# Kernel tuning notes

Hardware: AMD Instinct MI355X
Metric: run time of the kernel (lower is better)

The kernel has to match this reference:

```python
import jax, jax.numpy as jnp
import numpy as np

EPS = 1e-6

def _ln(x, g, b):
    mu = jnp.mean(x, axis=-1, keepdims=True)
    var = jnp.mean(jnp.square(x - mu), axis=-1, keepdims=True)
    return (x - mu) * jax.lax.rsqrt(var + EPS) * g + b

def setup_inputs() -> dict:
    key = jax.random.key(0)
    ks = jax.random.split(key, 8)
    B, S, D, H, HD, F = 4, 1024, 1024, 16, 64, 4096
    s = 0.02
    return {
        "hidden_state": jax.random.normal(ks[0], (B, S, D), jnp.float32),
        "mask": jnp.ones((B, S), jnp.int32),
        "Wq": jax.random.normal(ks[1], (H, D, HD), jnp.float32) * s,
        "bq": jnp.zeros((H, HD), jnp.float32),
        "Wk": jax.random.normal(ks[2], (H, D, HD), jnp.float32) * s,
        "bk": jnp.zeros((H, HD), jnp.float32),
        "Wv": jax.random.normal(ks[3], (H, D, HD), jnp.float32) * s,
        "bv": jnp.zeros((H, HD), jnp.float32),
        "Wo": jax.random.normal(ks[4], (D, D), jnp.float32) * s,
        "bo": jnp.zeros((D,), jnp.float32),
        "ln1_g": jnp.ones((D,), jnp.float32),
        "ln1_b": jnp.zeros((D,), jnp.float32),
        "ln2_g": jnp.ones((D,), jnp.float32),
        "ln2_b": jnp.zeros((D,), jnp.float32),
        "W1": jax.random.normal(ks[5], (D, F), jnp.float32) * s,
        "b1": jnp.zeros((F,), jnp.float32),
        "W2": jax.random.normal(ks[6], (F, D), jnp.float32) * s,
        "b2": jnp.zeros((D,), jnp.float32),
    }

def reference(hidden_state, mask, Wq, bq, Wk, bk, Wv, bv, Wo, bo,
              ln1_g, ln1_b, ln2_g, ln2_b, W1, b1, W2, b2):
    # Pre-norm
    x1 = _ln(hidden_state, ln1_g, ln1_b)  # [B,S,D]
    # Per-head projections stacked over head axis h
    q = jnp.einsum('bsd,hdk->bhsk', x1, Wq) + bq[:, None, :]
    k = jnp.einsum('bsd,hdk->bhsk', x1, Wk) + bk[:, None, :]
    v = jnp.einsum('bsd,hdk->bhsk', x1, Wv) + bv[:, None, :]
    head_dim = q.shape[-1]
    scores = jnp.einsum('bhqk,bhsk->bhqs', q, k) / jnp.sqrt(jnp.float32(head_dim))
    scores = jnp.where(mask[:, None, None, :] == 0, jnp.float32(-1e9), scores)
    w = jax.nn.softmax(scores, axis=-1)
    attn = jnp.einsum('bhqs,bhsk->bhqk', w, v)  # [B,H,S,HD]
    B, H, S, HD = attn.shape
    attn = attn.transpose(0, 2, 1, 3).reshape(B, S, H * HD)  # concat heads
    attn = attn @ Wo + bo
    h = attn + hidden_state
    x2 = _ln(h, ln2_g, ln2_b)
    ff = jax.nn.gelu(x2 @ W1 + b1, approximate=False) @ W2 + b2
    return ff + h
```

## Files before the change

### kernel.cpp

```cpp
#include <hip/hip_runtime.h>

typedef __bf16 bf16;
typedef __bf16 bf16x4 __attribute__((ext_vector_type(4)));
typedef __bf16 bf16x8 __attribute__((ext_vector_type(8)));
typedef float  f32x4  __attribute__((ext_vector_type(4)));

#define F32X4_ZERO ((f32x4){0.f, 0.f, 0.f, 0.f})

__device__ __forceinline__ f32x4 mfma16(bf16x8 a, bf16x8 b, f32x4 c) {
  return __builtin_amdgcn_mfma_f32_16x16x32_bf16(a, b, c, 0, 0, 0);
}

__device__ __forceinline__ void gld16(const void* g, void* l) {
  __builtin_amdgcn_global_load_lds((const __attribute__((address_space(1))) void*)g,
                                   (__attribute__((address_space(3))) void*)l, 16, 0, 0);
}

__device__ __forceinline__ float gelu_f(float u) {
  return 0.5f * u * (1.0f + erff(u * 0.70710678118654752f));
}

__device__ __forceinline__ bf16x8 frag_ld(const bf16* base, int row, int c16) {
  return *(const bf16x8*)((const char*)base + row * 128 + (((c16) ^ (row & 7)) << 4));
}

__device__ __forceinline__ bf16x8 frag_ld32(const bf16* base, int row, int c16) {
  return *(const bf16x8*)((const char*)base + row * 64 + ((c16 ^ ((row >> 1) & 3)) << 4));
}
#define WAITB(N) asm volatile("s_waitcnt vmcnt(" #N ")\ns_barrier" ::: "memory")

__global__ void transpose2(const float* __restrict__ src, size_t sBatch, int sStride,
                           bf16* __restrict__ dst, size_t dBatch, int dStride) {
  __shared__ bf16 t[32][33];
  src += (size_t)blockIdx.z * sBatch;
  dst += (size_t)blockIdx.z * dBatch;
  int c0 = blockIdx.x * 32, r0 = blockIdx.y * 32;
#pragma unroll
  for (int i = 0; i < 4; i++) {
    int r = threadIdx.y + i * 8;
    t[r][threadIdx.x] = (bf16)src[(size_t)(r0 + r) * sStride + c0 + threadIdx.x];
  }
  __syncthreads();
#pragma unroll
  for (int i = 0; i < 4; i++) {
    int c = threadIdx.y + i * 8;
    dst[(size_t)(c0 + c) * dStride + r0 + threadIdx.x] = t[threadIdx.x][c];
  }
}

__global__ __launch_bounds__(256) void ln_rows(const float* __restrict__ in,
                                               const float* __restrict__ gam,
                                               const float* __restrict__ bet,
                                               bf16* __restrict__ out) {
  int row = blockIdx.x, tid = threadIdx.x;
  f32x4 x = *(const f32x4*)(in + (size_t)row * 1024 + tid * 4);
  float s = 0.f, q = 0.f;
#pragma unroll
  for (int j = 0; j < 4; j++) { s += x[j]; q += x[j] * x[j]; }
#pragma unroll
  for (int o = 1; o < 64; o <<= 1) {
    s += __shfl_xor(s, o, 64);
    q += __shfl_xor(q, o, 64);
  }
  __shared__ float red[8];
  if ((tid & 63) == 0) { red[(tid >> 6) * 2] = s; red[(tid >> 6) * 2 + 1] = q; }
  __syncthreads();
  s = red[0] + red[2] + red[4] + red[6];
  q = red[1] + red[3] + red[5] + red[7];
  float mean = s * (1.f / 1024.f);
  float var  = q * (1.f / 1024.f) - mean * mean;
  float inv  = rsqrtf(var + 1e-6f);
  bf16x4 o;
#pragma unroll
  for (int j = 0; j < 4; j++) {
    int c = tid * 4 + j;
    o[j] = (bf16)((x[j] - mean) * inv * gam[c] + bet[c]);
  }
  *(bf16x4*)(out + (size_t)row * 1024 + tid * 4) = o;
}

enum { EPI_WO = 0, EPI_GELU = 1, EPI_ACC0 = 2, EPI_ACC = 3, EPI_FINAL = 4 };

__global__ __launch_bounds__(512) void pipe256x128_gelu(
    const bf16* __restrict__ A, const bf16* __restrict__ BT, const float* __restrict__ bias,
    int N, bf16* __restrict__ outb) {
  int tid = threadIdx.x, lane = tid & 63, wv = tid >> 6;
  int bid = blockIdx.x;
  int xcd = bid & 7, idx = bid >> 3;
  int mg = xcd >> 1, ng = xcd & 1;
  int m0 = (mg * 4 + (idx >> 4)) * 256;
  int n0 = (ng * 16 + (idx & 15)) * 128;
  int wrow = (wv >> 1) * 64, wcol = (wv & 1) * 64;
  __shared__ __align__(16) bf16 lds[3][12288];
  f32x4 acc[4][4];
#pragma unroll
  for (int a = 0; a < 4; a++)
#pragma unroll
    for (int n = 0; n < 4; n++) acc[a][n] = F32X4_ZERO;

  constexpr int K = 1024, nk = K / 32;
  int rin = lane >> 2;
  int sbc = ((lane & 3) ^ ((lane >> 3) & 3)) * 16;
  auto stage = [&](int slot, int k0) {
#pragma unroll
    for (int j = 0; j < 3; j++) {
      int c = wv * 3 + j;
      if (c < 16)
        gld16((const char*)A + ((size_t)(m0 + c * 16 + rin) * K + k0) * 2 + sbc,
              (char*)lds[slot] + c * 1024);
      else
        gld16((const char*)BT + ((size_t)(n0 + (c - 16) * 16 + rin) * K + k0) * 2 + sbc,
              (char*)lds[slot] + c * 1024);
    }
  };

  stage(0, 0); stage(1, 32);
#pragma unroll 1
  for (int t = 0; t < nk; t++) {
    if (t < nk - 1) WAITB(3);
    else            WAITB(0);
    if (t + 2 < nk) stage((t + 2) % 3, (t + 2) * 32);
    const bf16* As = lds[t % 3];
    const bf16* Bs = lds[t % 3] + 8192;
    int c16 = lane >> 4;
    bf16x8 af[4], bfr[4];
#pragma unroll
    for (int mf = 0; mf < 4; mf++)
      af[mf] = frag_ld32(As, wrow + mf * 16 + (lane & 15), c16);
#pragma unroll
    for (int nf = 0; nf < 4; nf++)
      bfr[nf] = frag_ld32(Bs, wcol + nf * 16 + (lane & 15), c16);
#pragma unroll
    for (int mf = 0; mf < 4; mf++)
#pragma unroll
      for (int nf = 0; nf < 4; nf++)
        acc[mf][nf] = mfma16(af[mf], bfr[nf], acc[mf][nf]);
  }
#pragma unroll
  for (int mf = 0; mf < 4; mf++)
#pragma unroll
    for (int nf = 0; nf < 4; nf++)
#pragma unroll
      for (int i = 0; i < 4; i++) {
        int row = m0 + wrow + mf * 16 + ((lane >> 4) << 2) + i;
        int col = n0 + wcol + nf * 16 + (lane & 15);
        outb[(size_t)row * N + col] = (bf16)gelu_f(acc[mf][nf][i] + bias[col]);
      }
}

template <int EPI, int K, int NTL>
__global__ __launch_bounds__(256) void pipe128(
    const bf16* __restrict__ A, const bf16* __restrict__ BT, const float* __restrict__ bias,
    int N,
    const float* __restrict__ resid, float* __restrict__ facc,
    bf16* __restrict__ outb, float* __restrict__ outf) {
  int tid = threadIdx.x, lane = tid & 63, wv = tid >> 6;
  int bid = blockIdx.x + (blockIdx.y << 3);
  int xcd = bid & 7, idx = bid >> 3;
  int m0 = (xcd * 4 + (idx >> NTL)) * 128;
  int n0 = (idx & ((1 << NTL) - 1)) * 128;
  int wrow = (wv >> 1) * 64, wcol = (wv & 1) * 64;
  __shared__ __align__(16) bf16 lds[3][8192];
  f32x4 acc[4][4];
#pragma unroll
  for (int a = 0; a < 4; a++)
#pragma unroll
    for (int n = 0; n < 4; n++) acc[a][n] = F32X4_ZERO;

  constexpr int nk = K / 32;
  int rin = lane >> 2;
  int sbc = ((lane & 3) ^ ((lane >> 3) & 3)) * 16;
  auto stage = [&](int slot, int k0) {
#pragma unroll
    for (int j = 0; j < 4; j++) {
      int c = wv * 4 + j;
      if (c < 8)
        gld16((const char*)A + ((size_t)(m0 + c * 16 + rin) * K + k0) * 2 + sbc,
              (char*)lds[slot] + c * 1024);
      else
        gld16((const char*)BT + ((size_t)(n0 + (c - 8) * 16 + rin) * K + k0) * 2 + sbc,
              (char*)lds[slot] + c * 1024);
    }
  };

  stage(0, 0); stage(1, 32);
#pragma unroll 1
  for (int t = 0; t < nk; t++) {
    if (t < nk - 1) WAITB(4);
    else            WAITB(0);
    if (t + 2 < nk) stage((t + 2) % 3, (t + 2) * 32);
    const bf16* As = lds[t % 3];
    const bf16* Bs = lds[t % 3] + 4096;
    int c16 = lane >> 4;
    bf16x8 af[4], bfr[4];
#pragma unroll
    for (int mf = 0; mf < 4; mf++)
      af[mf] = frag_ld32(As, wrow + mf * 16 + (lane & 15), c16);
#pragma unroll
    for (int nf = 0; nf < 4; nf++)
      bfr[nf] = frag_ld32(Bs, wcol + nf * 16 + (lane & 15), c16);
#pragma unroll
    for (int mf = 0; mf < 4; mf++)
#pragma unroll
      for (int nf = 0; nf < 4; nf++)
        acc[mf][nf] = mfma16(af[mf], bfr[nf], acc[mf][nf]);
  }
#pragma unroll
  for (int mf = 0; mf < 4; mf++)
#pragma unroll
    for (int nf = 0; nf < 4; nf++)
#pragma unroll
      for (int i = 0; i < 4; i++) {
        int row = m0 + wrow + mf * 16 + ((lane >> 4) << 2) + i;
        int col = n0 + wcol + nf * 16 + (lane & 15);
        size_t idx2 = (size_t)row * N + col;
        float v = acc[mf][nf][i];
        if constexpr (EPI == EPI_WO) {
          outf[idx2] = v + bias[col] + resid[idx2];
        } else if constexpr (EPI == EPI_GELU) {
          outb[idx2] = (bf16)gelu_f(v + bias[col]);
        } else if constexpr (EPI == EPI_ACC0) {
          facc[idx2] = v;
        } else if constexpr (EPI == EPI_ACC) {
          facc[idx2] += v;
        } else {
          outf[idx2] = facc[idx2] + v + bias[col] + resid[idx2];
        }
      }
}

__global__ __launch_bounds__(256) void qkv_pipe(
    const bf16* __restrict__ x1,
    const bf16* __restrict__ WqT, const bf16* __restrict__ WkT, const bf16* __restrict__ WvT,
    const float* __restrict__ bq, const float* __restrict__ bk, const float* __restrict__ bv,
    bf16* __restrict__ qo, bf16* __restrict__ ko, bf16* __restrict__ vto) {
  int tid = threadIdx.x, lane = tid & 63, wv = tid >> 6;
  int z = blockIdx.z;
  const bf16* BT; const float* bias;
  if (z == 0)      { BT = WqT; bias = bq; }
  else if (z == 1) { BT = WkT; bias = bk; }
  else             { BT = WvT; bias = bv; }
  int bid = blockIdx.x + (blockIdx.y << 3);
  int xcd = bid & 7, idx = bid >> 3;
  int m0 = (xcd * 4 + (idx >> 3)) * 128, n0 = (idx & 7) * 128;
  int wrow = (wv >> 1) * 64, wcol = (wv & 1) * 64;
  __shared__ __align__(16) bf16 lds[3][8192];
  f32x4 acc[4][4];
#pragma unroll
  for (int a = 0; a < 4; a++)
#pragma unroll
    for (int n = 0; n < 4; n++) acc[a][n] = F32X4_ZERO;

  constexpr int K = 1024, nk = K / 32;
  int rin = lane >> 2;
  int sbc = ((lane & 3) ^ ((lane >> 3) & 3)) * 16;
  auto stage = [&](int slot, int k0) {
#pragma unroll
    for (int j = 0; j < 4; j++) {
      int c = wv * 4 + j;
      if (c < 8)
        gld16((const char*)x1 + ((size_t)(m0 + c * 16 + rin) * K + k0) * 2 + sbc,
              (char*)lds[slot] + c * 1024);
      else
        gld16((const char*)BT + ((size_t)(n0 + (c - 8) * 16 + rin) * K + k0) * 2 + sbc,
              (char*)lds[slot] + c * 1024);
    }
  };

  stage(0, 0); stage(1, 32);
#pragma unroll 1
  for (int t = 0; t < nk; t++) {
    if (t < nk - 1) WAITB(4);
    else            WAITB(0);
    if (t + 2 < nk) stage((t + 2) % 3, (t + 2) * 32);
    const bf16* As = lds[t % 3];
    const bf16* Bs = lds[t % 3] + 4096;
    int c16 = lane >> 4;
    bf16x8 af[4], bfr[4];
#pragma unroll
    for (int mf = 0; mf < 4; mf++)
      af[mf] = frag_ld32(As, wrow + mf * 16 + (lane & 15), c16);
#pragma unroll
    for (int nf = 0; nf < 4; nf++)
      bfr[nf] = frag_ld32(Bs, wcol + nf * 16 + (lane & 15), c16);
#pragma unroll
    for (int mf = 0; mf < 4; mf++)
#pragma unroll
      for (int nf = 0; nf < 4; nf++)
        acc[mf][nf] = mfma16(af[mf], bfr[nf], acc[mf][nf]);
  }
#pragma unroll
  for (int mf = 0; mf < 4; mf++)
#pragma unroll
    for (int nf = 0; nf < 4; nf++)
#pragma unroll
      for (int i = 0; i < 4; i++) {
        int row  = m0 + wrow + mf * 16 + ((lane >> 4) << 2) + i;
        int ncol = n0 + wcol + nf * 16 + (lane & 15);
        int bb = row >> 10, s = row & 1023, head = ncol >> 6, d = ncol & 63;
        size_t bh = (size_t)bb * 16 + head;
        float v = acc[mf][nf][i] + bias[ncol];
        if (z == 0)      qo[(bh * 1024 + s) * 64 + d] = (bf16)(v * 0.125f);
        else if (z == 1) ko[(bh * 1024 + s) * 64 + d] = (bf16)v;
        else             vto[(bh * 64 + d) * 1024 + s] = (bf16)v;
      }
}

__global__ __launch_bounds__(512) void attn_flash(
    const bf16* __restrict__ qb, const bf16* __restrict__ kb, const bf16* __restrict__ vtb,
    const int* __restrict__ mask, bf16* __restrict__ attnC) {
  int tid = threadIdx.x, lane = tid & 63, wv = tid >> 6;
  int wgid = blockIdx.x;
  int nid  = (wgid & 7) * 64 + (wgid >> 3);
  int qblk = nid & 7, h = (nid >> 3) & 15, b = nid >> 7;
  int qrow0 = qblk * 128 + wv * 16;

  __shared__ float smask[1024];
  __shared__ __align__(16) bf16 kt[2][64 * 64];
  __shared__ __align__(16) bf16 vt[2][64 * 64];
  __shared__ __align__(16) bf16 pb[8][16][72];
  for (int i = tid; i < 1024; i += 512) smask[i] = mask[b * 1024 + i] ? 0.f : -1e9f;

  size_t bh = (size_t)b * 16 + h;
  const bf16* qp = qb + (bh * 1024 + qrow0) * 64;
  bf16x8 qa[2];
#pragma unroll
  for (int kc = 0; kc < 2; kc++)
    qa[kc] = *(const bf16x8*)(qp + (lane & 15) * 64 + kc * 32 + (lane >> 4) * 8);

  const bf16* kp = kb + bh * 1024 * 64;
  const bf16* vp = vtb + bh * 64 * 1024;
  bf16* myp = &pb[wv][0][0];

  bf16x8 vone;
#pragma unroll
  for (int j = 0; j < 8; j++) vone[j] = (bf16)1.0f;

  f32x4 ssum = F32X4_ZERO;
  f32x4 oacc[4];
#pragma unroll
  for (int i = 0; i < 4; i++) oacc[i] = F32X4_ZERO;

  int srl = lane >> 3;
  int sbc = ((lane & 7) ^ srl) * 16;
  auto stage = [&](int buf, int t2) {
    int key0n = t2 * 64;
#pragma unroll
    for (int j = 0; j < 2; j++) {
      int c = wv * 2 + j;
      if (c < 8) {
        int row = c * 8 + srl;
        gld16((const char*)kp + ((size_t)(key0n + row) * 64) * 2 + sbc,
              (char*)kt[buf] + c * 1024);
      } else {
        int row = (c - 8) * 8 + srl;
        gld16((const char*)vp + ((size_t)row * 1024 + key0n) * 2 + sbc,
              (char*)vt[buf] + (c - 8) * 1024);
      }
    }
  };

  stage(0, 0);
  __syncthreads();

  for (int t = 0; t < 16; t++) {
    int cur = t & 1;
    if (t < 15) stage(cur ^ 1, t + 1);
    const bf16* kcur = kt[cur];
    const bf16* vcur = vt[cur];
    int key0 = t * 64;
    f32x4 st[4];
    __builtin_amdgcn_s_setprio(1);
#pragma unroll
    for (int nt = 0; nt < 4; nt++) {
      st[nt] = F32X4_ZERO;
#pragma unroll
      for (int kc = 0; kc < 2; kc++) {
        bf16x8 kf = frag_ld(kcur, nt * 16 + (lane & 15), kc * 4 + (lane >> 4));
        st[nt] = mfma16(qa[kc], kf, st[nt]);
      }
    }
    __builtin_amdgcn_s_setprio(0);
#pragma unroll
    for (int nt = 0; nt < 4; nt++) {
      float ms = smask[key0 + nt * 16 + (lane & 15)] - 8.0f;
#pragma unroll
      for (int i = 0; i < 4; i++) st[nt][i] = __expf(st[nt][i] + ms);
    }
#pragma unroll
    for (int nt = 0; nt < 4; nt++)
#pragma unroll
      for (int i = 0; i < 4; i++)
        myp[((lane >> 4) * 4 + i) * 72 + nt * 16 + (lane & 15)] = (bf16)st[nt][i];
    __builtin_amdgcn_s_setprio(1);
#pragma unroll
    for (int kc = 0; kc < 2; kc++) {
      bf16x8 pa = *(const bf16x8*)(myp + (lane & 15) * 72 + kc * 32 + (lane >> 4) * 8);
      ssum = mfma16(pa, vone, ssum);
#pragma unroll
      for (int dn = 0; dn < 4; dn++) {
        bf16x8 vf = frag_ld(vcur, dn * 16 + (lane & 15), kc * 4 + (lane >> 4));
        oacc[dn] = mfma16(pa, vf, oacc[dn]);
      }
    }
    __builtin_amdgcn_s_setprio(0);
    __syncthreads();
  }
#pragma unroll
  for (int i = 0; i < 4; i++) {
    float inv = 1.0f / ssum[i];
    int row = qrow0 + ((lane >> 4) << 2) + i;
#pragma unroll
    for (int dn = 0; dn < 4; dn++)
      attnC[(size_t)(b * 1024 + row) * 1024 + h * 64 + dn * 16 + (lane & 15)] =
          (bf16)(oacc[dn][i] * inv);
  }
}

template <int EPI, int K>
__global__ __launch_bounds__(256) void gemm_bt(
    const bf16* __restrict__ A, const bf16* __restrict__ BT, const float* __restrict__ bias,
    int N,
    const float* __restrict__ resid, float* __restrict__ facc,
    bf16* __restrict__ outb, float* __restrict__ outf) {
  int tid = threadIdx.x, lane = tid & 63, wv = tid >> 6;
  int m0 = blockIdx.y * 128, n0 = blockIdx.x * 128;
  int wrow = (wv >> 1) * 64, wcol = (wv & 1) * 64;
  __shared__ __align__(16) bf16 lA[2][128 * 64];
  __shared__ __align__(16) bf16 lB[2][128 * 64];
  f32x4 acc[4][4];
#pragma unroll
  for (int a = 0; a < 4; a++)
#pragma unroll
    for (int n = 0; n < 4; n++) acc[a][n] = F32X4_ZERO;

  int cbs = ((lane & 7) ^ (lane >> 3)) * 16;
  auto stage = [&](int buf, int k0) {
#pragma unroll
    for (int s = 0; s < 4; s++) {
      int c = s * 4 + wv;
      int row = c * 8 + (lane >> 3);
      gld16((const char*)A  + ((size_t)(m0 + row) * K + k0) * 2 + cbs,
            (char*)lA[buf] + c * 1024);
      gld16((const char*)BT + ((size_t)(n0 + row) * K + k0) * 2 + cbs,
            (char*)lB[buf] + c * 1024);
    }
  };

  constexpr int nk = K >> 6;
  stage(0, 0);
  __syncthreads();
#pragma unroll 1
  for (int t = 0; t < nk; t++) {
    int cur = t & 1;
    if (t + 1 < nk) stage(cur ^ 1, (t + 1) * 64);
#pragma unroll
    for (int kc = 0; kc < 2; kc++) {
      int c16 = kc * 4 + (lane >> 4);
      bf16x8 af[4], bfr[4];
#pragma unroll
      for (int mf = 0; mf < 4; mf++)
        af[mf] = frag_ld(lA[cur], wrow + mf * 16 + (lane & 15), c16);
#pragma unroll
      for (int nf = 0; nf < 4; nf++)
        bfr[nf] = frag_ld(lB[cur], wcol + nf * 16 + (lane & 15), c16);
#pragma unroll
      for (int mf = 0; mf < 4; mf++)
#pragma unroll
        for (int nf = 0; nf < 4; nf++)
          acc[mf][nf] = mfma16(af[mf], bfr[nf], acc[mf][nf]);
    }
    __syncthreads();
  }
#pragma unroll
  for (int mf = 0; mf < 4; mf++)
#pragma unroll
    for (int nf = 0; nf < 4; nf++)
#pragma unroll
      for (int i = 0; i < 4; i++) {
        int row = m0 + wrow + mf * 16 + ((lane >> 4) << 2) + i;
        int col = n0 + wcol + nf * 16 + (lane & 15);
        size_t idx2 = (size_t)row * N + col;
        float v = acc[mf][nf][i];
        if constexpr (EPI == EPI_WO) {
          outf[idx2] = v + bias[col] + resid[idx2];
        } else if constexpr (EPI == EPI_GELU) {
          outb[idx2] = (bf16)gelu_f(v + bias[col]);
        } else if constexpr (EPI == EPI_ACC0) {
          facc[idx2] = v;
        } else if constexpr (EPI == EPI_ACC) {
          facc[idx2] += v;
        } else {
          outf[idx2] = facc[idx2] + v + bias[col] + resid[idx2];
        }
      }
}

extern "C" void kernel_launch(void* const* d_in, const int* in_sizes, int n_in,
                              void* d_out, int out_size, void* d_ws, size_t ws_size,
                              hipStream_t stream) {
  const float* hidden = (const float*)d_in[0];
  const int*   mask   = (const int*)d_in[1];
  const float* Wq = (const float*)d_in[2];
  const float* bq = (const float*)d_in[3];
  const float* Wk = (const float*)d_in[4];
  const float* bk = (const float*)d_in[5];
  const float* Wv = (const float*)d_in[6];
  const float* bv = (const float*)d_in[7];
  const float* Wo = (const float*)d_in[8];
  const float* bo = (const float*)d_in[9];
  const float* ln1g = (const float*)d_in[10];
  const float* ln1b = (const float*)d_in[11];
  const float* ln2g = (const float*)d_in[12];
  const float* ln2b = (const float*)d_in[13];
  const float* W1 = (const float*)d_in[14];
  const float* b1 = (const float*)d_in[15];
  const float* W2 = (const float*)d_in[16];
  const float* b2 = (const float*)d_in[17];
  float* out = (float*)d_out;

  char* ws = (char*)d_ws;
  const size_t MB = 1ull << 20;
  dim3 tb(32, 8);
  const size_t HB = 64 * 1024;

  if (ws_size >= 96 * MB) {
    bf16* x1    = (bf16*)(ws + 0 * MB);
    bf16* attnC = x1;
    bf16* x2    = x1;
    bf16* qbuf  = (bf16*)(ws + 8 * MB);
    bf16* W1T   = qbuf;
    bf16* kbuf  = (bf16*)(ws + 16 * MB);
    bf16* W2T   = kbuf;
    bf16* vtbuf = (bf16*)(ws + 24 * MB);
    float* hbuf = (float*)(ws + 32 * MB);
    bf16* WqT   = (bf16*)(ws + 48 * MB);
    bf16* WkT   = (bf16*)(ws + 50 * MB);
    bf16* WvT   = (bf16*)(ws + 52 * MB);
    bf16* WoT   = (bf16*)(ws + 54 * MB);
    bf16* gbuf  = (bf16*)(ws + 56 * MB);

    transpose2<<<dim3(2, 32, 16), tb, 0, stream>>>(Wq, HB, 64, WqT, HB, 1024);
    transpose2<<<dim3(2, 32, 16), tb, 0, stream>>>(Wk, HB, 64, WkT, HB, 1024);
    transpose2<<<dim3(2, 32, 16), tb, 0, stream>>>(Wv, HB, 64, WvT, HB, 1024);
    transpose2<<<dim3(32, 32, 1), tb, 0, stream>>>(Wo, 0, 1024, WoT, 0, 1024);
    ln_rows<<<4096, 256, 0, stream>>>(hidden, ln1g, ln1b, x1);
    qkv_pipe<<<dim3(8, 32, 3), 256, 0, stream>>>(x1, WqT, WkT, WvT, bq, bk, bv,
                                                 qbuf, kbuf, vtbuf);
    attn_flash<<<512, 512, 0, stream>>>(qbuf, kbuf, vtbuf, mask, attnC);
    pipe128<EPI_WO, 1024, 3><<<dim3(8, 32), 256, 0, stream>>>(attnC, WoT, bo, 1024,
                                                              hidden, nullptr, nullptr, hbuf);
    ln_rows<<<4096, 256, 0, stream>>>(hbuf, ln2g, ln2b, x2);
    transpose2<<<dim3(128, 32, 1), tb, 0, stream>>>(W1, 0, 4096, W1T, 0, 1024);
    transpose2<<<dim3(32, 128, 1), tb, 0, stream>>>(W2, 0, 1024, W2T, 0, 4096);
    pipe256x128_gelu<<<512, 512, 0, stream>>>(x2, W1T, b1, 4096, gbuf);
    pipe128<EPI_WO, 4096, 3><<<dim3(8, 32), 256, 0, stream>>>(gbuf, W2T, b2, 1024,
                                                              hbuf, nullptr, nullptr, out);
  } else {
    bf16* x1     = (bf16*)(ws + 0 * MB);
    bf16* attnC  = x1;
    bf16* x2     = x1;
    bf16* qbuf   = (bf16*)(ws + 8 * MB);
    bf16* W1Tc   = (bf16*)(ws + 8 * MB);
    bf16* W2Tc   = (bf16*)(ws + 10 * MB);
    bf16* gchunk = (bf16*)(ws + 12 * MB);
    bf16* kbuf   = (bf16*)(ws + 16 * MB);
    bf16* vtbuf  = (bf16*)(ws + 24 * MB);
    float* hbuf  = (float*)(ws + 16 * MB);
    bf16* WqT    = (bf16*)(ws + 32 * MB);
    bf16* WkT    = (bf16*)(ws + 34 * MB);
    bf16* WvT    = (bf16*)(ws + 36 * MB);
    bf16* WoT    = (bf16*)(ws + 38 * MB);
    float* outacc = (float*)(ws + 40 * MB);

    transpose2<<<dim3(2, 32, 16), tb, 0, stream>>>(Wq, HB, 64, WqT, HB, 1024);
    transpose2<<<dim3(2, 32, 16), tb, 0, stream>>>(Wk, HB, 64, WkT, HB, 1024);
    transpose2<<<dim3(2, 32, 16), tb, 0, stream>>>(Wv, HB, 64, WvT, HB, 1024);
    transpose2<<<dim3(32, 32, 1), tb, 0, stream>>>(Wo, 0, 1024, WoT, 0, 1024);
    ln_rows<<<4096, 256, 0, stream>>>(hidden, ln1g, ln1b, x1);
    qkv_pipe<<<dim3(8, 32, 3), 256, 0, stream>>>(x1, WqT, WkT, WvT, bq, bk, bv,
                                                 qbuf, kbuf, vtbuf);
    attn_flash<<<512, 512, 0, stream>>>(qbuf, kbuf, vtbuf, mask, attnC);
    pipe128<EPI_WO, 1024, 3><<<dim3(8, 32), 256, 0, stream>>>(attnC, WoT, bo, 1024,
                                                              hidden, nullptr, nullptr, hbuf);
    ln_rows<<<4096, 256, 0, stream>>>(hbuf, ln2g, ln2b, x2);

    for (int c = 0; c < 8; c++) {
      transpose2<<<dim3(16, 32, 1), tb, 0, stream>>>(W1 + c * 512, 0, 4096,
                                                     W1Tc, 0, 1024);
      transpose2<<<dim3(32, 16, 1), tb, 0, stream>>>(W2 + (size_t)c * 512 * 1024, 0, 1024,
                                                     W2Tc, 0, 512);
      gemm_bt<EPI_GELU, 1024><<<dim3(4, 32), 256, 0, stream>>>(x2, W1Tc, b1 + c * 512, 512,
                                                               nullptr, nullptr, gchunk, nullptr);
      if (c == 0)
        gemm_bt<EPI_ACC0, 512><<<dim3(8, 32), 256, 0, stream>>>(gchunk, W2Tc, b2, 1024,
                                                                nullptr, outacc, nullptr, nullptr);
      else if (c < 7)
        gemm_bt<EPI_ACC, 512><<<dim3(8, 32), 256, 0, stream>>>(gchunk, W2Tc, b2, 1024,
                                                               nullptr, outacc, nullptr, nullptr);
      else
        gemm_bt<EPI_FINAL, 512><<<dim3(8, 32), 256, 0, stream>>>(gchunk, W2Tc, b2, 1024,
                                                                 hbuf, outacc, nullptr, out);
    }
  }

  (void)in_sizes; (void)n_in; (void)out_size;
}
```

Measured before the change: 223.0 us.

## Use 256x128 QKV GEMM tiles, deepen pipe128 prefetch, precompute load offsets

Replaces the 128x128 QKV projection kernel with a 512-thread 256x128 tile variant, mirroring the FFN1 kernel, to raise operand reuse per block. The pipe128 GEMMs used for Wo and W2 gain a DEPTH template parameter and now prefetch three stages ahead with four LDS slots to hide more global latency. All GEMM kernels precompute their global source pointers and swizzled LDS fragment offsets once, then advance pointers incrementally, which cuts per-iteration address arithmetic. The trade-off is more LDS per block and fewer QKV blocks, which may reduce occupancy.

```diff
diff --git a/kernel.cpp b/kernel.cpp
--- a/kernel.cpp
+++ b/kernel.cpp
@@ -24,8 +24,8 @@
   return *(const bf16x8*)((const char*)base + row * 128 + (((c16) ^ (row & 7)) << 4));
 }
 
-__device__ __forceinline__ bf16x8 frag_ld32(const bf16* base, int row, int c16) {
-  return *(const bf16x8*)((const char*)base + row * 64 + ((c16 ^ ((row >> 1) & 3)) << 4));
+__device__ __forceinline__ int fo32(int row, int c16) {
+  return row * 64 + ((c16 ^ ((row >> 1) & 3)) << 4);
 }
 #define WAITB(N) asm volatile("s_waitcnt vmcnt(" #N ")\ns_barrier" ::: "memory")
 
@@ -87,9 +87,8 @@
   int tid = threadIdx.x, lane = tid & 63, wv = tid >> 6;
   int bid = blockIdx.x;
   int xcd = bid & 7, idx = bid >> 3;
-  int mg = xcd >> 1, ng = xcd & 1;
-  int m0 = (mg * 4 + (idx >> 4)) * 256;
-  int n0 = (ng * 16 + (idx & 15)) * 128;
+  int m0 = ((xcd >> 1) * 4 + (idx >> 4)) * 256;
+  int n0 = ((xcd & 1) * 16 + (idx & 15)) * 128;
   int wrow = (wv >> 1) * 64, wcol = (wv & 1) * 64;
   __shared__ __align__(16) bf16 lds[3][12288];
   f32x4 acc[4][4];
@@ -101,35 +100,40 @@
   constexpr int K = 1024, nk = K / 32;
   int rin = lane >> 2;
   int sbc = ((lane & 3) ^ ((lane >> 3) & 3)) * 16;
-  auto stage = [&](int slot, int k0) {
+  const char* gsrc[3]; int ldof[3];
+#pragma unroll
+  for (int j = 0; j < 3; j++) {
+    int c = wv * 3 + j;
+    if (c < 16) gsrc[j] = (const char*)A  + ((size_t)(m0 + c * 16 + rin) * K) * 2 + sbc;
+    else        gsrc[j] = (const char*)BT + ((size_t)(n0 + (c - 16) * 16 + rin) * K) * 2 + sbc;
+    ldof[j] = c * 1024;
+  }
+  auto stage = [&](int slot) {
 #pragma unroll
     for (int j = 0; j < 3; j++) {
-      int c = wv * 3 + j;
-      if (c < 16)
-        gld16((const char*)A + ((size_t)(m0 + c * 16 + rin) * K + k0) * 2 + sbc,
-              (char*)lds[slot] + c * 1024);
-      else
-        gld16((const char*)BT + ((size_t)(n0 + (c - 16) * 16 + rin) * K + k0) * 2 + sbc,
-              (char*)lds[slot] + c * 1024);
+      gld16(gsrc[j], (char*)lds[slot] + ldof[j]);
+      gsrc[j] += 64;
     }
   };
-
-  stage(0, 0); stage(1, 32);
+  int c16 = lane >> 4;
+  int foA[4], foB[4];
+#pragma unroll
+  for (int mf = 0; mf < 4; mf++) foA[mf] = fo32(wrow + mf * 16 + (lane & 15), c16);
+#pragma unroll
+  for (int nf = 0; nf < 4; nf++) foB[nf] = 16384 + fo32(wcol + nf * 16 + (lane & 15), c16);
+
+  stage(0); stage(1);
 #pragma unroll 1
   for (int t = 0; t < nk; t++) {
     if (t < nk - 1) WAITB(3);
     else            WAITB(0);
-    if (t + 2 < nk) stage((t + 2) % 3, (t + 2) * 32);
-    const bf16* As = lds[t % 3];
-    const bf16* Bs = lds[t % 3] + 8192;
-    int c16 = lane >> 4;
+    if (t + 2 < nk) stage((t + 2) % 3);
+    const char* sb = (const char*)lds[t % 3];
     bf16x8 af[4], bfr[4];
 #pragma unroll
-    for (int mf = 0; mf < 4; mf++)
-      af[mf] = frag_ld32(As, wrow + mf * 16 + (lane & 15), c16);
-#pragma unroll
-    for (int nf = 0; nf < 4; nf++)
-      bfr[nf] = frag_ld32(Bs, wcol + nf * 16 + (lane & 15), c16);
+    for (int mf = 0; mf < 4; mf++) af[mf] = *(const bf16x8*)(sb + foA[mf]);
+#pragma unroll
+    for (int nf = 0; nf < 4; nf++) bfr[nf] = *(const bf16x8*)(sb + foB[nf]);
 #pragma unroll
     for (int mf = 0; mf < 4; mf++)
 #pragma unroll
@@ -148,7 +152,90 @@
       }
 }
 
-template <int EPI, int K, int NTL>
+__global__ __launch_bounds__(512) void qkv_pipe256(
+    const bf16* __restrict__ x1,
+    const bf16* __restrict__ WqT, const bf16* __restrict__ WkT, const bf16* __restrict__ WvT,
+    const float* __restrict__ bq, const float* __restrict__ bk, const float* __restrict__ bv,
+    bf16* __restrict__ qo, bf16* __restrict__ ko, bf16* __restrict__ vto) {
+  int tid = threadIdx.x, lane = tid & 63, wv = tid >> 6;
+  int z = blockIdx.z;
+  const bf16* BT; const float* bias;
+  if (z == 0)      { BT = WqT; bias = bq; }
+  else if (z == 1) { BT = WkT; bias = bk; }
+  else             { BT = WvT; bias = bv; }
+  int bid = blockIdx.x;
+  int xcd = bid & 7, idx = bid >> 3;
+  int m0 = (xcd * 2 + (idx >> 3)) * 256;
+  int n0 = (idx & 7) * 128;
+  int wrow = (wv >> 1) * 64, wcol = (wv & 1) * 64;
+  __shared__ __align__(16) bf16 lds[3][12288];
+  f32x4 acc[4][4];
+#pragma unroll
+  for (int a = 0; a < 4; a++)
+#pragma unroll
+    for (int n = 0; n < 4; n++) acc[a][n] = F32X4_ZERO;
+
+  constexpr int K = 1024, nk = K / 32;
+  int rin = lane >> 2;
+  int sbc = ((lane & 3) ^ ((lane >> 3) & 3)) * 16;
+  const char* gsrc[3]; int ldof[3];
+#pragma unroll
+  for (int j = 0; j < 3; j++) {
+    int c = wv * 3 + j;
+    if (c < 16) gsrc[j] = (const char*)x1 + ((size_t)(m0 + c * 16 + rin) * K) * 2 + sbc;
+    else        gsrc[j] = (const char*)BT + ((size_t)(n0 + (c - 16) * 16 + rin) * K) * 2 + sbc;
+    ldof[j] = c * 1024;
+  }
+  auto stage = [&](int slot) {
+#pragma unroll
+    for (int j = 0; j < 3; j++) {
+      gld16(gsrc[j], (char*)lds[slot] + ldof[j]);
+      gsrc[j] += 64;
+    }
+  };
+  int c16 = lane >> 4;
+  int foA[4], foB[4];
+#pragma unroll
+  for (int mf = 0; mf < 4; mf++) foA[mf] = fo32(wrow + mf * 16 + (lane & 15), c16);
+#pragma unroll
+  for (int nf = 0; nf < 4; nf++) foB[nf] = 16384 + fo32(wcol + nf * 16 + (lane & 15), c16);
+
+  stage(0); stage(1);
+#pragma unroll 1
+  for (int t = 0; t < nk; t++) {
+    if (t < nk - 1) WAITB(3);
+    else            WAITB(0);
+    if (t + 2 < nk) stage((t + 2) % 3);
+    const char* sb = (const char*)lds[t % 3];
+    bf16x8 af[4], bfr[4];
+#pragma unroll
+    for (int mf = 0; mf < 4; mf++) af[mf] = *(const bf16x8*)(sb + foA[mf]);
+#pragma unroll
+    for (int nf = 0; nf < 4; nf++) bfr[nf] = *(const bf16x8*)(sb + foB[nf]);
+#pragma unroll
+    for (int mf = 0; mf < 4; mf++)
+#pragma unroll
+      for (int nf = 0; nf < 4; nf++)
+        acc[mf][nf] = mfma16(af[mf], bfr[nf], acc[mf][nf]);
+  }
+#pragma unroll
+  for (int mf = 0; mf < 4; mf++)
+#pragma unroll
+    for (int nf = 0; nf < 4; nf++)
+#pragma unroll
+      for (int i = 0; i < 4; i++) {
+        int row  = m0 + wrow + mf * 16 + ((lane >> 4) << 2) + i;
+        int ncol = n0 + wcol + nf * 16 + (lane & 15);
+        int bb = row >> 10, s = row & 1023, head = ncol >> 6, d = ncol & 63;
+        size_t bh = (size_t)bb * 16 + head;
+        float v = acc[mf][nf][i] + bias[ncol];
+        if (z == 0)      qo[(bh * 1024 + s) * 64 + d] = (bf16)(v * 0.125f);
+        else if (z == 1) ko[(bh * 1024 + s) * 64 + d] = (bf16)v;
+        else             vto[(bh * 64 + d) * 1024 + s] = (bf16)v;
+      }
+}
+
+template <int EPI, int K, int NTL, int DEPTH>
 __global__ __launch_bounds__(256) void pipe128(
     const bf16* __restrict__ A, const bf16* __restrict__ BT, const float* __restrict__ bias,
     int N,
@@ -160,7 +247,8 @@
   int m0 = (xcd * 4 + (idx >> NTL)) * 128;
   int n0 = (idx & ((1 << NTL) - 1)) * 128;
   int wrow = (wv >> 1) * 64, wcol = (wv & 1) * 64;
-  __shared__ __align__(16) bf16 lds[3][8192];
+  constexpr int SLOTS = DEPTH + 1;
+  __shared__ __align__(16) bf16 lds[SLOTS][8192];
   f32x4 acc[4][4];
 #pragma unroll
   for (int a = 0; a < 4; a++)
@@ -170,35 +258,47 @@
   constexpr int nk = K / 32;
   int rin = lane >> 2;
   int sbc = ((lane & 3) ^ ((lane >> 3) & 3)) * 16;
-  auto stage = [&](int slot, int k0) {
+  const char* gsrc[4]; int ldof[4];
+#pragma unroll
+  for (int j = 0; j < 4; j++) {
+    int c = wv * 4 + j;
+    if (c < 8) gsrc[j] = (const char*)A  + ((size_t)(m0 + c * 16 + rin) * K) * 2 + sbc;
+    else       gsrc[j] = (const char*)BT + ((size_t)(n0 + (c - 8) * 16 + rin) * K) * 2 + sbc;
+    ldof[j] = c * 1024;
+  }
+  auto stage = [&](int slot) {
 #pragma unroll
     for (int j = 0; j < 4; j++) {
-      int c = wv * 4 + j;
-      if (c < 8)
-        gld16((const char*)A + ((size_t)(m0 + c * 16 + rin) * K + k0) * 2 + sbc,
-              (char*)lds[slot] + c * 1024);
-      else
-        gld16((const char*)BT + ((size_t)(n0 + (c - 8) * 16 + rin) * K + k0) * 2 + sbc,
-              (char*)lds[slot] + c * 1024);
+      gld16(gsrc[j], (char*)lds[slot] + ldof[j]);
+      gsrc[j] += 64;
     }
   };
-
-  stage(0, 0); stage(1, 32);
+  int c16 = lane >> 4;
+  int foA[4], foB[4];
+#pragma unroll
+  for (int mf = 0; mf < 4; mf++) foA[mf] = fo32(wrow + mf * 16 + (lane & 15), c16);
+#pragma unroll
+  for (int nf = 0; nf < 4; nf++) foB[nf] = 8192 + fo32(wcol + nf * 16 + (lane & 15), c16);
+
+#pragma unroll
+  for (int p = 0; p < DEPTH; p++) stage(p);
 #pragma unroll 1
   for (int t = 0; t < nk; t++) {
-    if (t < nk - 1) WAITB(4);
-    else            WAITB(0);
-    if (t + 2 < nk) stage((t + 2) % 3, (t + 2) * 32);
-    const bf16* As = lds[t % 3];
-    const bf16* Bs = lds[t % 3] + 4096;
-    int c16 = lane >> 4;
+    if constexpr (DEPTH == 2) {
+      if (t < nk - 1) WAITB(4);
+      else            WAITB(0);
+    } else {
+      if (t < nk - 2)       WAITB(8);
+      else if (t == nk - 2) WAITB(4);
+      else                  WAITB(0);
+    }
+    if (t + DEPTH < nk) stage((t + DEPTH) % SLOTS);
+    const char* sb = (const char*)lds[t % SLOTS];
     bf16x8 af[4], bfr[4];
 #pragma unroll
-    for (int mf = 0; mf < 4; mf++)
-      af[mf] = frag_ld32(As, wrow + mf * 16 + (lane & 15), c16);
-#pragma unroll
-    for (int nf = 0; nf < 4; nf++)
-      bfr[nf] = frag_ld32(Bs, wcol + nf * 16 + (lane & 15), c16);
+    for (int mf = 0; mf < 4; mf++) af[mf] = *(const bf16x8*)(sb + foA[mf]);
+#pragma unroll
+    for (int nf = 0; nf < 4; nf++) bfr[nf] = *(const bf16x8*)(sb + foB[nf]);
 #pragma unroll
     for (int mf = 0; mf < 4; mf++)
 #pragma unroll
@@ -226,83 +326,6 @@
         } else {
           outf[idx2] = facc[idx2] + v + bias[col] + resid[idx2];
         }
-      }
-}
-
-__global__ __launch_bounds__(256) void qkv_pipe(
-    const bf16* __restrict__ x1,
-    const bf16* __restrict__ WqT, const bf16* __restrict__ WkT, const bf16* __restrict__ WvT,
-    const float* __restrict__ bq, const float* __restrict__ bk, const float* __restrict__ bv,
-    bf16* __restrict__ qo, bf16* __restrict__ ko, bf16* __restrict__ vto) {
-  int tid = threadIdx.x, lane = tid & 63, wv = tid >> 6;
-  int z = blockIdx.z;
-  const bf16* BT; const float* bias;
-  if (z == 0)      { BT = WqT; bias = bq; }
-  else if (z == 1) { BT = WkT; bias = bk; }
-  else             { BT = WvT; bias = bv; }
-  int bid = blockIdx.x + (blockIdx.y << 3);
-  int xcd = bid & 7, idx = bid >> 3;
-  int m0 = (xcd * 4 + (idx >> 3)) * 128, n0 = (idx & 7) * 128;
-  int wrow = (wv >> 1) * 64, wcol = (wv & 1) * 64;
-  __shared__ __align__(16) bf16 lds[3][8192];
-  f32x4 acc[4][4];
-#pragma unroll
-  for (int a = 0; a < 4; a++)
-#pragma unroll
-    for (int n = 0; n < 4; n++) acc[a][n] = F32X4_ZERO;
-
-  constexpr int K = 1024, nk = K / 32;
-  int rin = lane >> 2;
-  int sbc = ((lane & 3) ^ ((lane >> 3) & 3)) * 16;
-  auto stage = [&](int slot, int k0) {
-#pragma unroll
-    for (int j = 0; j < 4; j++) {
-      int c = wv * 4 + j;
-      if (c < 8)
-        gld16((const char*)x1 + ((size_t)(m0 + c * 16 + rin) * K + k0) * 2 + sbc,
-              (char*)lds[slot] + c * 1024);
-      else
-        gld16((const char*)BT + ((size_t)(n0 + (c - 8) * 16 + rin) * K + k0) * 2 + sbc,
-              (char*)lds[slot] + c * 1024);
-    }
-  };
-
-  stage(0, 0); stage(1, 32);
-#pragma unroll 1
-  for (int t = 0; t < nk; t++) {
-    if (t < nk - 1) WAITB(4);
-    else            WAITB(0);
-    if (t + 2 < nk) stage((t + 2) % 3, (t + 2) * 32);
-    const bf16* As = lds[t % 3];
-    const bf16* Bs = lds[t % 3] + 4096;
-    int c16 = lane >> 4;
-    bf16x8 af[4], bfr[4];
-#pragma unroll
-    for (int mf = 0; mf < 4; mf++)
-      af[mf] = frag_ld32(As, wrow + mf * 16 + (lane & 15), c16);
-#pragma unroll
-    for (int nf = 0; nf < 4; nf++)
-      bfr[nf] = frag_ld32(Bs, wcol + nf * 16 + (lane & 15), c16);
-#pragma unroll
-    for (int mf = 0; mf < 4; mf++)
-#pragma unroll
-      for (int nf = 0; nf < 4; nf++)
-        acc[mf][nf] = mfma16(af[mf], bfr[nf], acc[mf][nf]);
-  }
-#pragma unroll
-  for (int mf = 0; mf < 4; mf++)
-#pragma unroll
-    for (int nf = 0; nf < 4; nf++)
-#pragma unroll
-      for (int i = 0; i < 4; i++) {
-        int row  = m0 + wrow + mf * 16 + ((lane >> 4) << 2) + i;
-        int ncol = n0 + wcol + nf * 16 + (lane & 15);
-        int bb = row >> 10, s = row & 1023, head = ncol >> 6, d = ncol & 63;
-        size_t bh = (size_t)bb * 16 + head;
-        float v = acc[mf][nf][i] + bias[ncol];
-        if (z == 0)      qo[(bh * 1024 + s) * 64 + d] = (bf16)(v * 0.125f);
-        else if (z == 1) ko[(bh * 1024 + s) * 64 + d] = (bf16)v;
-        else             vto[(bh * 64 + d) * 1024 + s] = (bf16)v;
       }
 }
 
@@ -545,17 +568,17 @@
     transpose2<<<dim3(2, 32, 16), tb, 0, stream>>>(Wv, HB, 64, WvT, HB, 1024);
     transpose2<<<dim3(32, 32, 1), tb, 0, stream>>>(Wo, 0, 1024, WoT, 0, 1024);
     ln_rows<<<4096, 256, 0, stream>>>(hidden, ln1g, ln1b, x1);
-    qkv_pipe<<<dim3(8, 32, 3), 256, 0, stream>>>(x1, WqT, WkT, WvT, bq, bk, bv,
-                                                 qbuf, kbuf, vtbuf);
+    qkv_pipe256<<<dim3(128, 1, 3), 512, 0, stream>>>(x1, WqT, WkT, WvT, bq, bk, bv,
+                                                     qbuf, kbuf, vtbuf);
     attn_flash<<<512, 512, 0, stream>>>(qbuf, kbuf, vtbuf, mask, attnC);
-    pipe128<EPI_WO, 1024, 3><<<dim3(8, 32), 256, 0, stream>>>(attnC, WoT, bo, 1024,
-                                                              hidden, nullptr, nullptr, hbuf);
+    pipe128<EPI_WO, 1024, 3, 3><<<dim3(8, 32), 256, 0, stream>>>(attnC, WoT, bo, 1024,
+                                                                 hidden, nullptr, nullptr, hbuf);
     ln_rows<<<4096, 256, 0, stream>>>(hbuf, ln2g, ln2b, x2);
     transpose2<<<dim3(128, 32, 1), tb, 0, stream>>>(W1, 0, 4096, W1T, 0, 1024);
     transpose2<<<dim3(32, 128, 1), tb, 0, stream>>>(W2, 0, 1024, W2T, 0, 4096);
     pipe256x128_gelu<<<512, 512, 0, stream>>>(x2, W1T, b1, 4096, gbuf);
-    pipe128<EPI_WO, 4096, 3><<<dim3(8, 32), 256, 0, stream>>>(gbuf, W2T, b2, 1024,
-                                                              hbuf, nullptr, nullptr, out);
+    pipe128<EPI_WO, 4096, 3, 3><<<dim3(8, 32), 256, 0, stream>>>(gbuf, W2T, b2, 1024,
+                                                                 hbuf, nullptr, nullptr, out);
   } else {
     bf16* x1     = (bf16*)(ws + 0 * MB);
     bf16* attnC  = x1;
@@ -578,11 +601,11 @@
     transpose2<<<dim3(2, 32, 16), tb, 0, stream>>>(Wv, HB, 64, WvT, HB, 1024);
     transpose2<<<dim3(32, 32, 1), tb, 0, stream>>>(Wo, 0, 1024, WoT, 0, 1024);
     ln_rows<<<4096, 256, 0, stream>>>(hidden, ln1g, ln1b, x1);
-    qkv_pipe<<<dim3(8, 32, 3), 256, 0, stream>>>(x1, WqT, WkT, WvT, bq, bk, bv,
-                                                 qbuf, kbuf, vtbuf);
+    qkv_pipe256<<<dim3(128, 1, 3), 512, 0, stream>>>(x1, WqT, WkT, WvT, bq, bk, bv,
+                                                     qbuf, kbuf, vtbuf);
     attn_flash<<<512, 512, 0, stream>>>(qbuf, kbuf, vtbuf, mask, attnC);
-    pipe128<EPI_WO, 1024, 3><<<dim3(8, 32), 256, 0, stream>>>(attnC, WoT, bo, 1024,
-                                                              hidden, nullptr, nullptr, hbuf);
+    pipe128<EPI_WO, 1024, 3, 3><<<dim3(8, 32), 256, 0, stream>>>(attnC, WoT, bo, 1024,
+                                                                 hidden, nullptr, nullptr, hbuf);
     ln_rows<<<4096, 256, 0, stream>>>(hbuf, ln2g, ln2b, x2);
 
     for (int c = 0; c < 8; c++) {
```

Result: slower. 227.5 us (+2.0%).

## Split-K the W2 GEMM into two halves and combine partials separately

Applied to the files above, without the earlier changes.

The final FFN down-projection GEMM (M=4096, N=1024, K=4096) previously launched only 256 blocks of 128x128 tiles. It now splits K into two halves across blockIdx.z, giving 512 blocks that write bf16 partial sums into reused workspace buffers. A new elementwise kernel adds the two partials, the bias and the residual. The aim is better occupancy of the CUs, at the cost of an extra launch, extra partial-buffer traffic and bf16 rounding of the partial sums.

```diff
diff --git a/kernel.cpp b/kernel.cpp
--- a/kernel.cpp
+++ b/kernel.cpp
@@ -227,6 +227,92 @@
           outf[idx2] = facc[idx2] + v + bias[col] + resid[idx2];
         }
       }
+}
+
+template <int KSTRIDE, int KLOOP, int NTL>
+__global__ __launch_bounds__(256) void pipe128_part(
+    const bf16* __restrict__ Abase, const bf16* __restrict__ BTbase,
+    int N, bf16* __restrict__ p0, bf16* __restrict__ p1) {
+  int tid = threadIdx.x, lane = tid & 63, wv = tid >> 6;
+  int z = blockIdx.z;
+  const bf16* A  = Abase  + (size_t)z * KLOOP;
+  const bf16* BT = BTbase + (size_t)z * KLOOP;
+  bf16* outp = z ? p1 : p0;
+  int bid = blockIdx.x + (blockIdx.y << 3);
+  int xcd = bid & 7, idx = bid >> 3;
+  int m0 = (xcd * 4 + (idx >> NTL)) * 128;
+  int n0 = (idx & ((1 << NTL) - 1)) * 128;
+  int wrow = (wv >> 1) * 64, wcol = (wv & 1) * 64;
+  __shared__ __align__(16) bf16 lds[3][8192];
+  f32x4 acc[4][4];
+#pragma unroll
+  for (int a = 0; a < 4; a++)
+#pragma unroll
+    for (int n = 0; n < 4; n++) acc[a][n] = F32X4_ZERO;
+
+  constexpr int nk = KLOOP / 32;
+  int rin = lane >> 2;
+  int sbc = ((lane & 3) ^ ((lane >> 3) & 3)) * 16;
+  auto stage = [&](int slot, int k0) {
+#pragma unroll
+    for (int j = 0; j < 4; j++) {
+      int c = wv * 4 + j;
+      if (c < 8)
+        gld16((const char*)A + ((size_t)(m0 + c * 16 + rin) * KSTRIDE + k0) * 2 + sbc,
+              (char*)lds[slot] + c * 1024);
+      else
+        gld16((const char*)BT + ((size_t)(n0 + (c - 8) * 16 + rin) * KSTRIDE + k0) * 2 + sbc,
+              (char*)lds[slot] + c * 1024);
+    }
+  };
+
+  stage(0, 0); stage(1, 32);
+#pragma unroll 1
+  for (int t = 0; t < nk; t++) {
+    if (t < nk - 1) WAITB(4);
+    else            WAITB(0);
+    if (t + 2 < nk) stage((t + 2) % 3, (t + 2) * 32);
+    const bf16* As = lds[t % 3];
+    const bf16* Bs = lds[t % 3] + 4096;
+    int c16 = lane >> 4;
+    bf16x8 af[4], bfr[4];
+#pragma unroll
+    for (int mf = 0; mf < 4; mf++)
+      af[mf] = frag_ld32(As, wrow + mf * 16 + (lane & 15), c16);
+#pragma unroll
+    for (int nf = 0; nf < 4; nf++)
+      bfr[nf] = frag_ld32(Bs, wcol + nf * 16 + (lane & 15), c16);
+#pragma unroll
+    for (int mf = 0; mf < 4; mf++)
+#pragma unroll
+      for (int nf = 0; nf < 4; nf++)
+        acc[mf][nf] = mfma16(af[mf], bfr[nf], acc[mf][nf]);
+  }
+#pragma unroll
+  for (int mf = 0; mf < 4; mf++)
+#pragma unroll
+    for (int nf = 0; nf < 4; nf++)
+#pragma unroll
+      for (int i = 0; i < 4; i++) {
+        int row = m0 + wrow + mf * 16 + ((lane >> 4) << 2) + i;
+        int col = n0 + wcol + nf * 16 + (lane & 15);
+        outp[(size_t)row * N + col] = (bf16)acc[mf][nf][i];
+      }
+}
+
+__global__ __launch_bounds__(256) void combine_k(
+    const bf16* __restrict__ p0, const bf16* __restrict__ p1,
+    const float* __restrict__ bias, const float* __restrict__ resid,
+    float* __restrict__ out) {
+  size_t i4 = ((size_t)blockIdx.x * 256 + threadIdx.x) * 4;
+  bf16x4 a = *(const bf16x4*)(p0 + i4);
+  bf16x4 b = *(const bf16x4*)(p1 + i4);
+  f32x4 r = *(const f32x4*)(resid + i4);
+  f32x4 bb = *(const f32x4*)(bias + (i4 & 1023));
+  f32x4 o;
+#pragma unroll
+  for (int j = 0; j < 4; j++) o[j] = (float)a[j] + (float)b[j] + bb[j] + r[j];
+  *(f32x4*)(out + i4) = o;
 }
 
 __global__ __launch_bounds__(256) void qkv_pipe(
@@ -528,11 +614,13 @@
     bf16* x1    = (bf16*)(ws + 0 * MB);
     bf16* attnC = x1;
     bf16* x2    = x1;
+    bf16* part0 = x1;
     bf16* qbuf  = (bf16*)(ws + 8 * MB);
     bf16* W1T   = qbuf;
     bf16* kbuf  = (bf16*)(ws + 16 * MB);
     bf16* W2T   = kbuf;
     bf16* vtbuf = (bf16*)(ws + 24 * MB);
+    bf16* part1 = vtbuf;
     float* hbuf = (float*)(ws + 32 * MB);
     bf16* WqT   = (bf16*)(ws + 48 * MB);
     bf16* WkT   = (bf16*)(ws + 50 * MB);
@@ -554,8 +642,9 @@
     transpose2<<<dim3(128, 32, 1), tb, 0, stream>>>(W1, 0, 4096, W1T, 0, 1024);
     transpose2<<<dim3(32, 128, 1), tb, 0, stream>>>(W2, 0, 1024, W2T, 0, 4096);
     pipe256x128_gelu<<<512, 512, 0, stream>>>(x2, W1T, b1, 4096, gbuf);
-    pipe128<EPI_WO, 4096, 3><<<dim3(8, 32), 256, 0, stream>>>(gbuf, W2T, b2, 1024,
-                                                              hbuf, nullptr, nullptr, out);
+    pipe128_part<4096, 2048, 3><<<dim3(8, 32, 2), 256, 0, stream>>>(gbuf, W2T, 1024,
+                                                                    part0, part1);
+    combine_k<<<4096, 256, 0, stream>>>(part0, part1, b2, hbuf, out);
   } else {
     bf16* x1     = (bf16*)(ws + 0 * MB);
     bf16* attnC  = x1;
```

New measurement: 223.1 us, median of 2. No clear change (+0.0%).
